# Kernel tuning notes

Hardware: AMD Instinct MI355X
Metric: run time of the kernel (lower is better)

Reference implementation:

```python
import jax, jax.numpy as jnp
import numpy as np

NUM_GROUPS = 32
EPS = 1e-6


def group_norm(x, w, b):
    # x: (B, C, L); normalize per group of C//32 channels over (channels-in-group, L)
    B, C, L = x.shape
    xg = x.reshape(B, NUM_GROUPS, C // NUM_GROUPS, L)
    mean = jnp.mean(xg, axis=(2, 3), keepdims=True)
    var = jnp.var(xg, axis=(2, 3), keepdims=True)
    xn = ((xg - mean) * jax.lax.rsqrt(var + EPS)).reshape(B, C, L)
    return xn * w[None, :, None] + b[None, :, None]


def conv1x1(x, w, b):
    # 1x1 Conv1d == channel-mixing linear. x: (B,C,L), w: (O,C), b: (O,)
    return jnp.einsum('oc,bcl->bol', w, x) + b[None, :, None]


def setup_inputs() -> dict:
    key = jax.random.key(0)
    ks = jax.random.split(key, 6)
    B, C, L = 8, 512, 2048
    s = 1.0 / np.sqrt(C)
    return {
        'x': jax.random.normal(ks[0], (B, C, L), dtype=jnp.float32),
        'gn_w': jnp.ones((C,), jnp.float32),
        'gn_b': jnp.zeros((C,), jnp.float32),
        'wq': jax.random.normal(ks[1], (C, C), dtype=jnp.float32) * s,
        'bq': jnp.zeros((C,), jnp.float32),
        'wk': jax.random.normal(ks[2], (C, C), dtype=jnp.float32) * s,
        'bk': jnp.zeros((C,), jnp.float32),
        'wv': jax.random.normal(ks[3], (C, C), dtype=jnp.float32) * s,
        'bv': jnp.zeros((C,), jnp.float32),
        'wo': jax.random.normal(ks[4], (C, C), dtype=jnp.float32) * s,
        'bo': jnp.zeros((C,), jnp.float32),
    }


def reference(x, gn_w, gn_b, wq, bq, wk, bk, wv, bv, wo, bo):
    B, C, L = x.shape
    h = group_norm(x, gn_w, gn_b)
    q = conv1x1(h, wq, bq)  # (B,C,L)
    k = conv1x1(h, wk, bk)
    v = conv1x1(h, wv, bv)
    scale = jnp.asarray(C, x.dtype) ** -0.5
    # scores over length: w[b,i,j] = sum_c q[b,c,i] k[b,c,j]
    w_ = jnp.einsum('bci,bcj->bij', q, k) * scale
    w_ = jax.nn.softmax(w_, axis=-1)
    # h[b,c,i] = sum_j w[b,i,j] v[b,c,j]
    h = jnp.einsum('bij,bcj->bci', w_, v)
    h = conv1x1(h, wo, bo)
    return x + h
```

## Files before the change

kernel.cpp:

```cpp
#include <hip/hip_runtime.h>
#include <math.h>

#define BATCH 8
#define CH 512
#define LEN 2048
#define NG 32
#define CPG 16

typedef unsigned short u16;
typedef __bf16 bf16x8 __attribute__((ext_vector_type(8)));
typedef float f32x4 __attribute__((ext_vector_type(4)));

__device__ __forceinline__ u16 f2bf(float f) {
    union { float f; unsigned u; } c; c.f = f;
    unsigned r = c.u + 0x7fffu + ((c.u >> 16) & 1u);
    return (u16)(r >> 16);
}
__device__ __forceinline__ float bf2f(u16 h) {
    union { unsigned u; float f; } c; c.u = ((unsigned)h) << 16;
    return c.f;
}
__device__ __forceinline__ void gload16(const u16* g, u16* l) {
    __builtin_amdgcn_global_load_lds(
        (const __attribute__((address_space(1))) unsigned int*)g,
        (__attribute__((address_space(3))) unsigned int*)l, 16, 0, 0);
}

__global__ __launch_bounds__(256) void zerof4(float4* __restrict__ p) {
    p[blockIdx.x * 256 + threadIdx.x] = make_float4(0.f, 0.f, 0.f, 0.f);
}

__global__ __launch_bounds__(256) void wconv4(const float* __restrict__ w0, const float* __restrict__ w1,
                                              const float* __restrict__ w2, const float* __restrict__ w3,
                                              u16* __restrict__ o0, u16* __restrict__ o1,
                                              u16* __restrict__ o2, u16* __restrict__ o3) {
    const float* s; u16* d;
    switch (blockIdx.y) {
        case 0: s = w0; d = o0; break;
        case 1: s = w1; d = o1; break;
        case 2: s = w2; d = o2; break;
        default: s = w3; d = o3; break;
    }
    const int i = blockIdx.x * 256 + threadIdx.x;
    float4 f = ((const float4*)s)[i];
    ushort4 o = make_ushort4(f2bf(f.x), f2bf(f.y), f2bf(f.z), f2bf(f.w));
    ((ushort4*)d)[i] = o;
}

__global__ __launch_bounds__(256) void gn_stats(const float* __restrict__ x,
                                                const float* __restrict__ gw,
                                                const float* __restrict__ gb,
                                                float* __restrict__ gnA,
                                                float* __restrict__ gnB) {
    const int b = blockIdx.x >> 5, g = blockIdx.x & 31;
    const float4* xp = (const float4*)(x + ((size_t)b * CH + (size_t)g * CPG) * LEN);
    float s = 0.f, s2 = 0.f;
    for (int i = threadIdx.x; i < (CPG * LEN) / 4; i += 256) {
        float4 v = xp[i];
        s += v.x + v.y + v.z + v.w;
        s2 = fmaf(v.x, v.x, fmaf(v.y, v.y, fmaf(v.z, v.z, fmaf(v.w, v.w, s2))));
    }
    #pragma unroll
    for (int off = 32; off > 0; off >>= 1) {
        s  += __shfl_down(s, off, 64);
        s2 += __shfl_down(s2, off, 64);
    }
    __shared__ float sm[2][4];
    const int lane = threadIdx.x & 63, wv = threadIdx.x >> 6;
    if (lane == 0) { sm[0][wv] = s; sm[1][wv] = s2; }
    __syncthreads();
    if (threadIdx.x < CPG) {
        const float S  = sm[0][0] + sm[0][1] + sm[0][2] + sm[0][3];
        const float S2 = sm[1][0] + sm[1][1] + sm[1][2] + sm[1][3];
        const float mean = S * (1.f / (CPG * LEN));
        const float var  = S2 * (1.f / (CPG * LEN)) - mean * mean;
        const float rstd = rsqrtf(var + 1e-6f);
        const int c = g * CPG + threadIdx.x;
        const float sc = rstd * gw[c];
        gnA[b * CH + c] = sc;
        gnB[b * CH + c] = gb[c] - mean * sc;
    }
}

__global__ __launch_bounds__(256) void gn_apply_t(const float* __restrict__ x,
                                                  const float* __restrict__ gnA,
                                                  const float* __restrict__ gnB,
                                                  u16* __restrict__ Ht) {
    __shared__ float tile[64][65];
    const int b = blockIdx.z, c0 = blockIdx.y * 64, l0 = blockIdx.x * 64;
    const int t = threadIdx.x, tl = t & 63, tr = t >> 6;
    #pragma unroll 4
    for (int i = 0; i < 16; ++i) {
        const int c = tr + i * 4;
        const float a = gnA[b * CH + c0 + c];
        const float sh = gnB[b * CH + c0 + c];
        tile[c][tl] = x[((size_t)b * CH + c0 + c) * LEN + l0 + tl] * a + sh;
    }
    __syncthreads();
    #pragma unroll 4
    for (int i = 0; i < 16; ++i) {
        const int l = tr + i * 4;
        Ht[((size_t)b * LEN + l0 + l) * CH + c0 + tl] = f2bf(tile[tl][l]);
    }
}

#define EPI_QK   0
#define EPI_TBN  1
#define EPI_EXP  2
#define EPI_TNRM 3
#define EPI_FIN  4

template <int MODE>
__global__ __launch_bounds__(256) void gemm_bt(
    const u16* __restrict__ A, int lda, long long sA,
    const u16* __restrict__ B, int ldb, long long sB,
    void* __restrict__ Out, void* __restrict__ Out2,
    int ldo, long long sO,
    const float* __restrict__ bias, const float* __restrict__ bias2,
    const float* __restrict__ res, long long sR,
    float* __restrict__ rsum, long long sRS,
    int K, float alpha) {
    __shared__ u16 As[128 * 32];
    __shared__ u16 Bs[128 * 32];
    const int b = blockIdx.z;
    const int n0 = blockIdx.x * 128, m0 = blockIdx.y * 128;
    A += (size_t)b * sA;
    B += (size_t)b * sB;
    const int t = threadIdx.x;
    const int lane = t & 63, wid = t >> 6;

    const int rowL = t >> 2, kq = t & 3;
    const u16* gA0 = A + (size_t)(m0 + rowL) * lda + kq * 8;
    const u16* gA1 = gA0 + (size_t)64 * lda;
    const u16* gB0 = B + (size_t)(n0 + rowL) * ldb + kq * 8;
    const u16* gB1 = gB0 + (size_t)64 * ldb;
    u16* lA0 = As + t * 8;
    u16* lA1 = As + 2048 + t * 8;
    u16* lB0 = Bs + t * 8;
    u16* lB1 = Bs + 2048 + t * 8;

    f32x4 acc[4][4];
    #pragma unroll
    for (int i = 0; i < 4; ++i)
        #pragma unroll
        for (int j = 0; j < 4; ++j)
            acc[i][j] = (f32x4){0.f, 0.f, 0.f, 0.f};

    const int mf = (wid & 1) * 64 + (lane & 15);
    const int nf = (wid >> 1) * 64 + (lane & 15);
    const int kf = (lane >> 4) * 8;

    for (int k0 = 0; k0 < K; k0 += 32) {
        gload16(gA0, lA0);
        gload16(gA1, lA1);
        gload16(gB0, lB0);
        gload16(gB1, lB1);
        gA0 += 32; gA1 += 32; gB0 += 32; gB1 += 32;
        __syncthreads();
        bf16x8 af[4], bfr[4];
        #pragma unroll
        for (int i = 0; i < 4; ++i) af[i]  = *(const bf16x8*)(As + (mf + i * 16) * 32 + kf);
        #pragma unroll
        for (int j = 0; j < 4; ++j) bfr[j] = *(const bf16x8*)(Bs + (nf + j * 16) * 32 + kf);
        #pragma unroll
        for (int i = 0; i < 4; ++i)
            #pragma unroll
            for (int j = 0; j < 4; ++j)
                acc[i][j] = __builtin_amdgcn_mfma_f32_16x16x32_bf16(af[i], bfr[j], acc[i][j], 0, 0, 0);
        __syncthreads();
    }

    const int quad = lane >> 4, col = lane & 15;
    const int wm = (wid & 1) * 64, wn = (wid >> 1) * 64;

    if (MODE == EPI_FIN) {
        float* O = (float*)Out + (size_t)b * sO;
        const float* R = res + (size_t)b * sR;
        #pragma unroll
        for (int i = 0; i < 4; ++i) {
            const int mb = m0 + wm + i * 16 + quad * 4;
            #pragma unroll
            for (int j = 0; j < 4; ++j) {
                const int n = n0 + wn + j * 16 + col;
                const float bb = bias[n];
                const size_t base = (size_t)n * ldo + mb;
                const float4 r4 = *(const float4*)&R[base];
                float4 o4;
                o4.x = acc[i][j][0] + bb + r4.x;
                o4.y = acc[i][j][1] + bb + r4.y;
                o4.z = acc[i][j][2] + bb + r4.z;
                o4.w = acc[i][j][3] + bb + r4.w;
                *(float4*)&O[base] = o4;
            }
        }
    } else if (MODE == EPI_EXP) {
        u16* O = (u16*)Out + (size_t)b * sO;
        float* RS = rsum + (size_t)b * sRS;
        float psum[4] = {0.f, 0.f, 0.f, 0.f};
        #pragma unroll
        for (int i = 0; i < 4; ++i) {
            const int mb = m0 + wm + i * 16 + quad * 4;
            #pragma unroll
            for (int j = 0; j < 4; ++j) {
                const int n = n0 + wn + j * 16 + col;
                u16 h0 = f2bf(__expf(acc[i][j][0] * alpha));
                u16 h1 = f2bf(__expf(acc[i][j][1] * alpha));
                u16 h2 = f2bf(__expf(acc[i][j][2] * alpha));
                u16 h3 = f2bf(__expf(acc[i][j][3] * alpha));
                psum[j] += bf2f(h0) + bf2f(h1) + bf2f(h2) + bf2f(h3);
                *(ushort4*)&O[(size_t)n * ldo + mb] = make_ushort4(h0, h1, h2, h3);
            }
        }
        #pragma unroll
        for (int j = 0; j < 4; ++j) {
            psum[j] += __shfl_xor(psum[j], 16, 64);
            psum[j] += __shfl_xor(psum[j], 32, 64);
        }
        if (quad == 0) {
            #pragma unroll
            for (int j = 0; j < 4; ++j)
                atomicAdd(&RS[n0 + wn + j * 16 + col], psum[j]);
        }
    } else {
        u16* O;
        const float* bi = bias;
        const float* RS = (MODE == EPI_TNRM) ? rsum + (size_t)b * sRS : nullptr;
        int mbase = m0 + wm;
        if (MODE == EPI_QK) {
            const bool hi = (m0 & 512) != 0;
            O  = (u16*)(hi ? Out2 : Out) + (size_t)b * sO;
            bi = hi ? bias2 : bias;
            mbase = (m0 & 511) + wm;
        } else {
            O = (u16*)Out + (size_t)b * sO;
        }
        #pragma unroll
        for (int i = 0; i < 4; ++i) {
            const int mb = mbase + i * 16 + quad * 4;
            float4 bm = make_float4(0.f, 0.f, 0.f, 0.f);
            if (MODE == EPI_QK) bm = *(const float4*)&bi[mb];
            #pragma unroll
            for (int j = 0; j < 4; ++j) {
                const int n = n0 + wn + j * 16 + col;
                float v0 = acc[i][j][0], v1 = acc[i][j][1], v2 = acc[i][j][2], v3 = acc[i][j][3];
                if (MODE == EPI_QK)  { v0 += bm.x; v1 += bm.y; v2 += bm.z; v3 += bm.w; }
                if (MODE == EPI_TBN) { const float bb = bi[n]; v0 += bb; v1 += bb; v2 += bb; v3 += bb; }
                if (MODE == EPI_TNRM) {
                    const float inv = 1.f / RS[n];
                    v0 *= inv; v1 *= inv; v2 *= inv; v3 *= inv;
                }
                ushort4 pk = make_ushort4(f2bf(v0), f2bf(v1), f2bf(v2), f2bf(v3));
                *(ushort4*)&O[(size_t)n * ldo + mb] = pk;
            }
        }
    }
}

extern "C" void kernel_launch(void* const* d_in, const int* in_sizes, int n_in,
                              void* d_out, int out_size, void* d_ws, size_t ws_size,
                              hipStream_t stream) {
    const float* x    = (const float*)d_in[0];
    const float* gn_w = (const float*)d_in[1];
    const float* gn_b = (const float*)d_in[2];
    const float* wq   = (const float*)d_in[3];
    const float* bq   = (const float*)d_in[4];
    const float* wk   = (const float*)d_in[5];
    const float* bk   = (const float*)d_in[6];
    const float* wv   = (const float*)d_in[7];
    const float* bv   = (const float*)d_in[8];
    const float* wo   = (const float*)d_in[9];
    const float* bo   = (const float*)d_in[10];
    float* out = (float*)d_out;

    char* p = (char*)d_ws;
    const size_t WSZ = (size_t)CH * CH * 2;
    const size_t HSZ = (size_t)BATCH * CH * LEN * 2;
    u16* Wqk = (u16*)p; p += 2 * WSZ;
    u16* Wvb = (u16*)p; p += WSZ;
    u16* Wob = (u16*)p; p += WSZ;
    u16* Ht  = (u16*)p; p += HSZ;
    u16* Qt  = (u16*)p; p += HSZ;
    u16* Kt  = (u16*)p; p += HSZ;
    u16* Vb  = (u16*)p; p += HSZ;
    u16* Sb  = (u16*)p; p += (size_t)BATCH * LEN * LEN * 2;
    float* gnA = (float*)p; p += (size_t)BATCH * CH * 4;
    float* gnB = (float*)p; p += (size_t)BATCH * CH * 4;
    float* rowsum = (float*)p;

    const long long sH = (long long)LEN * CH;
    const long long sV = (long long)CH * LEN;
    const long long sS = (long long)LEN * LEN;
    const float scale = 0.04419417382415922f;

    wconv4<<<dim3(256, 4), 256, 0, stream>>>(wq, wk, wv, wo,
                                             Wqk, Wqk + (size_t)CH * CH, Wvb, Wob);
    gn_stats<<<BATCH * NG, 256, 0, stream>>>(x, gn_w, gn_b, gnA, gnB);
    gn_apply_t<<<dim3(LEN / 64, CH / 64, BATCH), 256, 0, stream>>>(x, gnA, gnB, Ht);
    zerof4<<<BATCH * LEN / 1024, 256, 0, stream>>>((float4*)rowsum);

    gemm_bt<EPI_QK><<<dim3(16, 8, 8), 256, 0, stream>>>(
        Wqk, CH, 0, Ht, CH, sH, Qt, Kt, CH, sH, bq, bk, nullptr, 0, nullptr, 0, CH, 0.f);
    gemm_bt<EPI_TBN><<<dim3(4, 16, 8), 256, 0, stream>>>(
        Ht, CH, sH, Wvb, CH, 0, Vb, nullptr, LEN, sV, bv, nullptr, nullptr, 0, nullptr, 0, CH, 0.f);
    gemm_bt<EPI_EXP><<<dim3(16, 16, 8), 256, 0, stream>>>(
        Kt, CH, sH, Qt, CH, sH, Sb, nullptr, LEN, sS, nullptr, nullptr, nullptr, 0, rowsum, LEN, CH, scale);
    gemm_bt<EPI_TNRM><<<dim3(16, 4, 8), 256, 0, stream>>>(
        Vb, LEN, sV, Sb, LEN, sS, Ht, nullptr, CH, sH, nullptr, nullptr, nullptr, 0, rowsum, LEN, LEN, 0.f);
    gemm_bt<EPI_FIN><<<dim3(4, 16, 8), 256, 0, stream>>>(
        Ht, CH, sH, Wob, CH, 0, out, nullptr, LEN, sV, bo, nullptr, x, sV, nullptr, 0, CH, 0.f);
}
```

Baseline: 330.1 us.

## Switch GEMM to 32x32x16 MFMA with 64-wide K tiles

Replaces the 16x16x32 bf16 MFMA tiling with 32x32x16 MFMA (2x2 per wave) and doubles the K step per iteration to 64, which halves the barrier count and raises the work done per LDS load. The epilogues are remapped to the 32x32 accumulator layout, and the softmax reciprocal is hoisted out of the inner loop. LDS rows are now 128 bytes wide with no padding, so the fragment reads may hit bank conflicts.

```diff
diff --git a/kernel.cpp b/kernel.cpp
--- a/kernel.cpp
+++ b/kernel.cpp
@@ -9,7 +9,7 @@
 
 typedef unsigned short u16;
 typedef __bf16 bf16x8 __attribute__((ext_vector_type(8)));
-typedef float f32x4 __attribute__((ext_vector_type(4)));
+typedef float f32x16 __attribute__((ext_vector_type(16)));
 
 __device__ __forceinline__ u16 f2bf(float f) {
     union { float f; unsigned u; } c; c.f = f;
@@ -120,8 +120,8 @@
     const float* __restrict__ res, long long sR,
     float* __restrict__ rsum, long long sRS,
     int K, float alpha) {
-    __shared__ u16 As[128 * 32];
-    __shared__ u16 Bs[128 * 32];
+    __shared__ u16 As[128 * 64];
+    __shared__ u16 Bs[128 * 64];
     const int b = blockIdx.z;
     const int n0 = blockIdx.x * 128, m0 = blockIdx.y * 128;
     A += (size_t)b * sA;
@@ -129,97 +129,101 @@
     const int t = threadIdx.x;
     const int lane = t & 63, wid = t >> 6;
 
-    const int rowL = t >> 2, kq = t & 3;
-    const u16* gA0 = A + (size_t)(m0 + rowL) * lda + kq * 8;
-    const u16* gA1 = gA0 + (size_t)64 * lda;
-    const u16* gB0 = B + (size_t)(n0 + rowL) * ldb + kq * 8;
-    const u16* gB1 = gB0 + (size_t)64 * ldb;
-    u16* lA0 = As + t * 8;
-    u16* lA1 = As + 2048 + t * 8;
-    u16* lB0 = Bs + t * 8;
-    u16* lB1 = Bs + 2048 + t * 8;
-
-    f32x4 acc[4][4];
+    const int rowL = t >> 3, kq = t & 7;
+    const u16* gA[4];
+    const u16* gB[4];
+    u16* lA[4];
+    u16* lB[4];
     #pragma unroll
-    for (int i = 0; i < 4; ++i)
-        #pragma unroll
-        for (int j = 0; j < 4; ++j)
-            acc[i][j] = (f32x4){0.f, 0.f, 0.f, 0.f};
-
-    const int mf = (wid & 1) * 64 + (lane & 15);
-    const int nf = (wid >> 1) * 64 + (lane & 15);
-    const int kf = (lane >> 4) * 8;
-
-    for (int k0 = 0; k0 < K; k0 += 32) {
-        gload16(gA0, lA0);
-        gload16(gA1, lA1);
-        gload16(gB0, lB0);
-        gload16(gB1, lB1);
-        gA0 += 32; gA1 += 32; gB0 += 32; gB1 += 32;
+    for (int g = 0; g < 4; ++g) {
+        gA[g] = A + (size_t)(m0 + rowL + g * 32) * lda + kq * 8;
+        gB[g] = B + (size_t)(n0 + rowL + g * 32) * ldb + kq * 8;
+        lA[g] = As + t * 8 + g * 2048;
+        lB[g] = Bs + t * 8 + g * 2048;
+    }
+
+    f32x16 acc[2][2];
+    #pragma unroll
+    for (int i = 0; i < 2; ++i)
+        #pragma unroll
+        for (int j = 0; j < 2; ++j)
+            acc[i][j] = (f32x16)(0.f);
+
+    const int col = lane & 31, half = lane >> 5;
+    const int wm = (wid & 1) * 64, wn = (wid >> 1) * 64;
+    const int mf = wm + col, nf = wn + col;
+    const int kb = half * 8;
+
+    for (int k0 = 0; k0 < K; k0 += 64) {
+        #pragma unroll
+        for (int g = 0; g < 4; ++g) {
+            gload16(gA[g], lA[g]);
+            gload16(gB[g], lB[g]);
+            gA[g] += 64; gB[g] += 64;
+        }
         __syncthreads();
-        bf16x8 af[4], bfr[4];
-        #pragma unroll
-        for (int i = 0; i < 4; ++i) af[i]  = *(const bf16x8*)(As + (mf + i * 16) * 32 + kf);
-        #pragma unroll
-        for (int j = 0; j < 4; ++j) bfr[j] = *(const bf16x8*)(Bs + (nf + j * 16) * 32 + kf);
-        #pragma unroll
-        for (int i = 0; i < 4; ++i)
-            #pragma unroll
-            for (int j = 0; j < 4; ++j)
-                acc[i][j] = __builtin_amdgcn_mfma_f32_16x16x32_bf16(af[i], bfr[j], acc[i][j], 0, 0, 0);
+        #pragma unroll
+        for (int ks = 0; ks < 4; ++ks) {
+            bf16x8 a0 = *(const bf16x8*)(As + (mf)      * 64 + ks * 16 + kb);
+            bf16x8 a1 = *(const bf16x8*)(As + (mf + 32) * 64 + ks * 16 + kb);
+            bf16x8 b0 = *(const bf16x8*)(Bs + (nf)      * 64 + ks * 16 + kb);
+            bf16x8 b1 = *(const bf16x8*)(Bs + (nf + 32) * 64 + ks * 16 + kb);
+            acc[0][0] = __builtin_amdgcn_mfma_f32_32x32x16_bf16(a0, b0, acc[0][0], 0, 0, 0);
+            acc[0][1] = __builtin_amdgcn_mfma_f32_32x32x16_bf16(a0, b1, acc[0][1], 0, 0, 0);
+            acc[1][0] = __builtin_amdgcn_mfma_f32_32x32x16_bf16(a1, b0, acc[1][0], 0, 0, 0);
+            acc[1][1] = __builtin_amdgcn_mfma_f32_32x32x16_bf16(a1, b1, acc[1][1], 0, 0, 0);
+        }
         __syncthreads();
     }
-
-    const int quad = lane >> 4, col = lane & 15;
-    const int wm = (wid & 1) * 64, wn = (wid >> 1) * 64;
 
     if (MODE == EPI_FIN) {
         float* O = (float*)Out + (size_t)b * sO;
         const float* R = res + (size_t)b * sR;
         #pragma unroll
-        for (int i = 0; i < 4; ++i) {
-            const int mb = m0 + wm + i * 16 + quad * 4;
+        for (int im = 0; im < 2; ++im)
             #pragma unroll
-            for (int j = 0; j < 4; ++j) {
-                const int n = n0 + wn + j * 16 + col;
-                const float bb = bias[n];
-                const size_t base = (size_t)n * ldo + mb;
-                const float4 r4 = *(const float4*)&R[base];
-                float4 o4;
-                o4.x = acc[i][j][0] + bb + r4.x;
-                o4.y = acc[i][j][1] + bb + r4.y;
-                o4.z = acc[i][j][2] + bb + r4.z;
-                o4.w = acc[i][j][3] + bb + r4.w;
-                *(float4*)&O[base] = o4;
+            for (int g4 = 0; g4 < 4; ++g4) {
+                const int mb = m0 + wm + im * 32 + g4 * 8 + half * 4;
+                #pragma unroll
+                for (int jn = 0; jn < 2; ++jn) {
+                    const int n = n0 + wn + jn * 32 + col;
+                    const float bb = bias[n];
+                    const size_t base = (size_t)n * ldo + mb;
+                    const float4 r4 = *(const float4*)&R[base];
+                    float4 o4;
+                    o4.x = acc[im][jn][g4 * 4 + 0] + bb + r4.x;
+                    o4.y = acc[im][jn][g4 * 4 + 1] + bb + r4.y;
+                    o4.z = acc[im][jn][g4 * 4 + 2] + bb + r4.z;
+                    o4.w = acc[im][jn][g4 * 4 + 3] + bb + r4.w;
+                    *(float4*)&O[base] = o4;
+                }
             }
-        }
     } else if (MODE == EPI_EXP) {
         u16* O = (u16*)Out + (size_t)b * sO;
         float* RS = rsum + (size_t)b * sRS;
-        float psum[4] = {0.f, 0.f, 0.f, 0.f};
-        #pragma unroll
-        for (int i = 0; i < 4; ++i) {
-            const int mb = m0 + wm + i * 16 + quad * 4;
+        float psum[2] = {0.f, 0.f};
+        #pragma unroll
+        for (int im = 0; im < 2; ++im)
             #pragma unroll
-            for (int j = 0; j < 4; ++j) {
-                const int n = n0 + wn + j * 16 + col;
-                u16 h0 = f2bf(__expf(acc[i][j][0] * alpha));
-                u16 h1 = f2bf(__expf(acc[i][j][1] * alpha));
-                u16 h2 = f2bf(__expf(acc[i][j][2] * alpha));
-                u16 h3 = f2bf(__expf(acc[i][j][3] * alpha));
-                psum[j] += bf2f(h0) + bf2f(h1) + bf2f(h2) + bf2f(h3);
-                *(ushort4*)&O[(size_t)n * ldo + mb] = make_ushort4(h0, h1, h2, h3);
+            for (int g4 = 0; g4 < 4; ++g4) {
+                const int mb = m0 + wm + im * 32 + g4 * 8 + half * 4;
+                #pragma unroll
+                for (int jn = 0; jn < 2; ++jn) {
+                    const int n = n0 + wn + jn * 32 + col;
+                    u16 h0 = f2bf(__expf(acc[im][jn][g4 * 4 + 0] * alpha));
+                    u16 h1 = f2bf(__expf(acc[im][jn][g4 * 4 + 1] * alpha));
+                    u16 h2 = f2bf(__expf(acc[im][jn][g4 * 4 + 2] * alpha));
+                    u16 h3 = f2bf(__expf(acc[im][jn][g4 * 4 + 3] * alpha));
+                    psum[jn] += bf2f(h0) + bf2f(h1) + bf2f(h2) + bf2f(h3);
+                    *(ushort4*)&O[(size_t)n * ldo + mb] = make_ushort4(h0, h1, h2, h3);
+                }
             }
-        }
-        #pragma unroll
-        for (int j = 0; j < 4; ++j) {
-            psum[j] += __shfl_xor(psum[j], 16, 64);
-            psum[j] += __shfl_xor(psum[j], 32, 64);
-        }
-        if (quad == 0) {
+        #pragma unroll
+        for (int jn = 0; jn < 2; ++jn) psum[jn] += __shfl_xor(psum[jn], 32, 64);
+        if (half == 0) {
             #pragma unroll
-            for (int j = 0; j < 4; ++j)
-                atomicAdd(&RS[n0 + wn + j * 16 + col], psum[j]);
+            for (int jn = 0; jn < 2; ++jn)
+                atomicAdd(&RS[n0 + wn + jn * 32 + col], psum[jn]);
         }
     } else {
         u16* O;
@@ -234,25 +238,32 @@
         } else {
             O = (u16*)Out + (size_t)b * sO;
         }
-        #pragma unroll
-        for (int i = 0; i < 4; ++i) {
-            const int mb = mbase + i * 16 + quad * 4;
-            float4 bm = make_float4(0.f, 0.f, 0.f, 0.f);
-            if (MODE == EPI_QK) bm = *(const float4*)&bi[mb];
+        float inv[2];
+        if (MODE == EPI_TNRM) {
+            inv[0] = 1.f / RS[n0 + wn + col];
+            inv[1] = 1.f / RS[n0 + wn + 32 + col];
+        }
+        #pragma unroll
+        for (int im = 0; im < 2; ++im)
             #pragma unroll
-            for (int j = 0; j < 4; ++j) {
-                const int n = n0 + wn + j * 16 + col;
-                float v0 = acc[i][j][0], v1 = acc[i][j][1], v2 = acc[i][j][2], v3 = acc[i][j][3];
-                if (MODE == EPI_QK)  { v0 += bm.x; v1 += bm.y; v2 += bm.z; v3 += bm.w; }
-                if (MODE == EPI_TBN) { const float bb = bi[n]; v0 += bb; v1 += bb; v2 += bb; v3 += bb; }
-                if (MODE == EPI_TNRM) {
-                    const float inv = 1.f / RS[n];
-                    v0 *= inv; v1 *= inv; v2 *= inv; v3 *= inv;
+            for (int g4 = 0; g4 < 4; ++g4) {
+                const int mb = mbase + im * 32 + g4 * 8 + half * 4;
+                float4 bm = make_float4(0.f, 0.f, 0.f, 0.f);
+                if (MODE == EPI_QK) bm = *(const float4*)&bi[mb];
+                #pragma unroll
+                for (int jn = 0; jn < 2; ++jn) {
+                    const int n = n0 + wn + jn * 32 + col;
+                    float v0 = acc[im][jn][g4 * 4 + 0];
+                    float v1 = acc[im][jn][g4 * 4 + 1];
+                    float v2 = acc[im][jn][g4 * 4 + 2];
+                    float v3 = acc[im][jn][g4 * 4 + 3];
+                    if (MODE == EPI_QK)  { v0 += bm.x; v1 += bm.y; v2 += bm.z; v3 += bm.w; }
+                    if (MODE == EPI_TBN) { const float bb = bi[n]; v0 += bb; v1 += bb; v2 += bb; v3 += bb; }
+                    if (MODE == EPI_TNRM) { v0 *= inv[jn]; v1 *= inv[jn]; v2 *= inv[jn]; v3 *= inv[jn]; }
+                    ushort4 pk = make_ushort4(f2bf(v0), f2bf(v1), f2bf(v2), f2bf(v3));
+                    *(ushort4*)&O[(size_t)n * ldo + mb] = pk;
                 }
-                ushort4 pk = make_ushort4(f2bf(v0), f2bf(v1), f2bf(v2), f2bf(v3));
-                *(ushort4*)&O[(size_t)n * ldo + mb] = pk;
             }
-        }
     }
 }
 
```

Result: slower. 369.7 us (+12.0%).
